# Performance work log

Measured on AMD Instinct MI355X. Metric: run time of the kernel, lower is better.

The kernel has to match this reference:

```python
import jax, jax.numpy as jnp
import numpy as np

K = 1_000_000      # number of sparse (2D-det, 3D-anchor) candidate pairs
ROWS = 200         # max 2D detections
COLS = 70400       # number of 3D anchors (200*176*2)
SENTINEL = -9999999.0


def setup_inputs() -> dict:
    key = jax.random.key(0)
    ks = jax.random.split(key, 12)
    input_1 = jax.random.normal(ks[0], (1, 4, 1, K), dtype=jnp.float32)
    idx0 = jax.random.randint(ks[1], (K,), 0, ROWS)
    idx1 = jax.random.randint(ks[2], (K,), 0, COLS)
    tensor_index = jnp.stack([idx0, idx1], axis=1).astype(jnp.int64)
    # fuse_2d_3d: 1x1 Conv2d stack 4->18->36->36->1 (weights as (out,in) matrices)
    def w(k, o, i):
        return jax.random.normal(k, (o, i), dtype=jnp.float32) * (1.0 / np.sqrt(i))
    return {
        "input_1": input_1,
        "tensor_index": tensor_index,
        "W1": w(ks[3], 18, 4),  "b1": jnp.zeros((18,), jnp.float32),
        "W2": w(ks[4], 36, 18), "b2": jnp.zeros((36,), jnp.float32),
        "W3": w(ks[5], 36, 36), "b3": jnp.zeros((36,), jnp.float32),
        "W4": w(ks[6], 1, 36),  "b4": jnp.zeros((1,), jnp.float32),
    }


def reference(input_1, tensor_index, W1, b1, W2, b2, W3, b3, W4, b4):
    # 1x1 convs over (1,4,1,K) are channel matmuls over the K pair axis.
    x = input_1[0, :, 0, :]                                   # (4, K)
    h = jax.nn.relu(jnp.dot(W1, x) + b1[:, None])             # (18, K)
    h = jax.nn.relu(jnp.dot(W2, h) + b2[:, None])             # (36, K)
    h = jax.nn.relu(jnp.dot(W3, h) + b3[:, None])             # (36, K)
    v = (jnp.dot(W4, h) + b4[:, None])[0]                     # (K,) fused score per pair
    # Scatter into dense sentinel-filled grid, then max-reduce the 200 dim
    # (equivalent to MaxPool2d([200,1]) in the original).
    dense = jnp.full((ROWS, COLS), SENTINEL, dtype=input_1.dtype)
    dense = dense.at[tensor_index[:, 0], tensor_index[:, 1]].max(v)
    out = jnp.max(dense, axis=0).reshape(1, -1, 1)            # (1, 70400, 1)
    flag = 1
    return (out, flag)
```

## Files before the change

### kernel.cpp

```cpp
#include <hip/hip_runtime.h>

#define KN 1000000
#define NCOLS 70400
#define NPAIRS (KN / 32)
#define NBLK 1024
#define NTHR 256

typedef _Float16 f16x8 __attribute__((ext_vector_type(8)));
typedef float    f32x4 __attribute__((ext_vector_type(4)));

__device__ __forceinline__ unsigned encodeF(float f) {
    unsigned b = __float_as_uint(f);
    return (b & 0x80000000u) ? ~b : (b | 0x80000000u);
}
__device__ __forceinline__ float decodeF(unsigned e) {
    unsigned b = (e & 0x80000000u) ? (e & 0x7fffffffu) : ~e;
    return __uint_as_float(b);
}
#define ENC_SENT 0x34E76980u

#define MFMA16(a, b, c) __builtin_amdgcn_mfma_f32_16x16x32_f16((a), (b), (c), 0, 0, 0)

#define OW1 0
#define OB1 72
#define OW2 90
#define OB2 738
#define OW3 774
#define OB3 2070
#define OW4 2106
#define OB4 2142
#define NWTS 2143


__global__ __launch_bounds__(NTHR)
__attribute__((amdgpu_waves_per_eu(4, 4)))
void mlp_scatter_mfma(const float* __restrict__ x, const int* __restrict__ tidx,
                      const float* __restrict__ W1, const float* __restrict__ b1,
                      const float* __restrict__ W2, const float* __restrict__ b2,
                      const float* __restrict__ W3, const float* __restrict__ b3,
                      const float* __restrict__ W4, const float* __restrict__ b4,
                      unsigned* __restrict__ outU)
{
    __shared__ float    sw[NWTS];
    __shared__ _Float16 smem[4][2][1152];

    const int t    = threadIdx.x;
    const int lane = t & 63;
    const int wv   = t >> 6;
    const int quad = lane >> 4;
    const int n    = lane & 15;

    for (int i = t; i < 72;   i += NTHR) sw[OW1 + i] = W1[i];
    for (int i = t; i < 18;   i += NTHR) sw[OB1 + i] = b1[i];
    for (int i = t; i < 648;  i += NTHR) sw[OW2 + i] = W2[i];
    for (int i = t; i < 36;   i += NTHR) sw[OB2 + i] = b2[i];
    for (int i = t; i < 1296; i += NTHR) sw[OW3 + i] = W3[i];
    for (int i = t; i < 36;   i += NTHR) sw[OB3 + i] = b3[i];
    for (int i = t; i < 36;   i += NTHR) sw[OW4 + i] = W4[i];
    if (t == 0) sw[OB4] = b4[0];

    _Float16* Ha = &smem[wv][0][0];
    _Float16* Hb = &smem[wv][1][0];

    for (int i = lane; i < 128; i += 64) {
        const int row = i >> 3, dc = i & 7;
        ((unsigned*)(Ha + row * 72 + 48))[dc] = 0u;
        ((unsigned*)(Hb + row * 72 + 48))[dc] = 0u;
    }
    __syncthreads();

    auto bf = [&](int off, int OUT, int IN, int tt, int ks) {
        f16x8 r;
#pragma unroll
        for (int j = 0; j < 8; ++j) {
            int k  = ks * 32 + quad * 8 + j;
            int ng = tt * 16 + n;
            float w = (ng < OUT && k < IN) ? sw[off + ng * IN + k] : 0.0f;
            r[j] = (_Float16)w;
        }
        return r;
    };
    const f16x8 B1_0 = bf(OW1, 18,  4, 0, 0), B1_1 = bf(OW1, 18,  4, 1, 0);
    const f16x8 B2_0 = bf(OW2, 36, 18, 0, 0), B2_1 = bf(OW2, 36, 18, 1, 0), B2_2 = bf(OW2, 36, 18, 2, 0);
    const f16x8 B3_00 = bf(OW3, 36, 36, 0, 0), B3_01 = bf(OW3, 36, 36, 0, 1);
    const f16x8 B3_10 = bf(OW3, 36, 36, 1, 0), B3_11 = bf(OW3, 36, 36, 1, 1);
    const f16x8 B3_20 = bf(OW3, 36, 36, 2, 0), B3_21 = bf(OW3, 36, 36, 2, 1);

    const float bias1_0 = sw[OB1 + n];
    const float bias1_1 = (n < 2) ? sw[OB1 + 16 + n] : 0.0f;
    const float bias2_0 = sw[OB2 + n], bias2_1 = sw[OB2 + 16 + n];
    const float bias2_2 = (n < 4) ? sw[OB2 + 32 + n] : 0.0f;
    const float bias3_0 = sw[OB3 + n], bias3_1 = sw[OB3 + 16 + n];
    const float bias3_2 = (n < 4) ? sw[OB3 + 32 + n] : 0.0f;
    const float b4s = sw[OB4];
    const float w4_0 = sw[OW4 + n], w4_1 = sw[OW4 + 16 + n];
    const float w4_2 = (n < 4) ? sw[OW4 + 32 + n] : 0.0f;

    const int gw = (blockIdx.x * blockDim.x + t) >> 6;
    const int nw = (gridDim.x * blockDim.x) >> 6;

    float cxa0, cxa1, cxa2, cxa3, cxb0, cxb1, cxb2, cxb3;
    int cca = 0, ccb = 0;
    if (gw < NPAIRS) {
        const int kb = gw * 32;
        cxa0 = x[0 * KN + kb + n];      cxb0 = x[0 * KN + kb + 16 + n];
        cxa1 = x[1 * KN + kb + n];      cxb1 = x[1 * KN + kb + 16 + n];
        cxa2 = x[2 * KN + kb + n];      cxb2 = x[2 * KN + kb + 16 + n];
        cxa3 = x[3 * KN + kb + n];      cxb3 = x[3 * KN + kb + 16 + n];
        cca  = tidx[2 * (kb + n) + 1];  ccb  = tidx[2 * (kb + 16 + n) + 1];
    }

    for (int p = gw; p < NPAIRS; ) {
        const int pn = p + nw;
        const float xa0 = cxa0, xa1 = cxa1, xa2 = cxa2, xa3 = cxa3;
        const float xb0 = cxb0, xb1 = cxb1, xb2 = cxb2, xb3 = cxb3;
        const int cola = cca, colb = ccb;
        if (pn < NPAIRS) {
            const int kb = pn * 32;
            cxa0 = x[0 * KN + kb + n];      cxb0 = x[0 * KN + kb + 16 + n];
            cxa1 = x[1 * KN + kb + n];      cxb1 = x[1 * KN + kb + 16 + n];
            cxa2 = x[2 * KN + kb + n];      cxb2 = x[2 * KN + kb + 16 + n];
            cxa3 = x[3 * KN + kb + n];      cxb3 = x[3 * KN + kb + 16 + n];
            cca  = tidx[2 * (kb + n) + 1];  ccb  = tidx[2 * (kb + 16 + n) + 1];
        }

        f16x8 a1a = {}, a1b = {};
        if (quad == 0) {
            a1a[0] = (_Float16)xa0; a1a[1] = (_Float16)xa1;
            a1a[2] = (_Float16)xa2; a1a[3] = (_Float16)xa3;
            a1b[0] = (_Float16)xb0; a1b[1] = (_Float16)xb1;
            a1b[2] = (_Float16)xb2; a1b[3] = (_Float16)xb3;
        }
        f32x4 c0a = {bias1_0, bias1_0, bias1_0, bias1_0};
        f32x4 c1a = {bias1_1, bias1_1, bias1_1, bias1_1};
        f32x4 c0b = c0a, c1b = c1a;
        c0a = MFMA16(a1a, B1_0, c0a);  c0b = MFMA16(a1b, B1_0, c0b);
        c1a = MFMA16(a1a, B1_1, c1a);  c1b = MFMA16(a1b, B1_1, c1b);
#pragma unroll
        for (int r = 0; r < 4; ++r) {
            const int row = (quad * 4 + r) * 72;
            Ha[row + n]      = (_Float16)fmaxf(c0a[r], 0.0f);
            Ha[row + 16 + n] = (_Float16)fmaxf(c1a[r], 0.0f);
            Hb[row + n]      = (_Float16)fmaxf(c0b[r], 0.0f);
            Hb[row + 16 + n] = (_Float16)fmaxf(c1b[r], 0.0f);
        }

        const f16x8 a2a = *(const f16x8*)&Ha[n * 72 + quad * 8];
        const f16x8 a2b = *(const f16x8*)&Hb[n * 72 + quad * 8];
        f32x4 d0a = {bias2_0, bias2_0, bias2_0, bias2_0};
        f32x4 d1a = {bias2_1, bias2_1, bias2_1, bias2_1};
        f32x4 d2a = {bias2_2, bias2_2, bias2_2, bias2_2};
        f32x4 d0b = d0a, d1b = d1a, d2b = d2a;
        d0a = MFMA16(a2a, B2_0, d0a);  d0b = MFMA16(a2b, B2_0, d0b);
        d1a = MFMA16(a2a, B2_1, d1a);  d1b = MFMA16(a2b, B2_1, d1b);
        d2a = MFMA16(a2a, B2_2, d2a);  d2b = MFMA16(a2b, B2_2, d2b);
#pragma unroll
        for (int r = 0; r < 4; ++r) {
            const int row = (quad * 4 + r) * 72;
            Ha[row + n]      = (_Float16)fmaxf(d0a[r], 0.0f);
            Ha[row + 16 + n] = (_Float16)fmaxf(d1a[r], 0.0f);
            Ha[row + 32 + n] = (_Float16)fmaxf(d2a[r], 0.0f);
            Hb[row + n]      = (_Float16)fmaxf(d0b[r], 0.0f);
            Hb[row + 16 + n] = (_Float16)fmaxf(d1b[r], 0.0f);
            Hb[row + 32 + n] = (_Float16)fmaxf(d2b[r], 0.0f);
        }

        const f16x8 a30a = *(const f16x8*)&Ha[n * 72 + quad * 8];
        const f16x8 a31a = *(const f16x8*)&Ha[n * 72 + 32 + quad * 8];
        const f16x8 a30b = *(const f16x8*)&Hb[n * 72 + quad * 8];
        const f16x8 a31b = *(const f16x8*)&Hb[n * 72 + 32 + quad * 8];
        f32x4 e0a = {bias3_0, bias3_0, bias3_0, bias3_0};
        f32x4 e1a = {bias3_1, bias3_1, bias3_1, bias3_1};
        f32x4 e2a = {bias3_2, bias3_2, bias3_2, bias3_2};
        f32x4 e0b = e0a, e1b = e1a, e2b = e2a;
        e0a = MFMA16(a30a, B3_00, e0a);  e0a = MFMA16(a31a, B3_01, e0a);
        e1a = MFMA16(a30a, B3_10, e1a);  e1a = MFMA16(a31a, B3_11, e1a);
        e2a = MFMA16(a30a, B3_20, e2a);  e2a = MFMA16(a31a, B3_21, e2a);
        e0b = MFMA16(a30b, B3_00, e0b);  e0b = MFMA16(a31b, B3_01, e0b);
        e1b = MFMA16(a30b, B3_10, e1b);  e1b = MFMA16(a31b, B3_11, e1b);
        e2b = MFMA16(a30b, B3_20, e2b);  e2b = MFMA16(a31b, B3_21, e2b);

        float pa[4], pb[4];
#pragma unroll
        for (int r = 0; r < 4; ++r) {
            pa[r] = fmaf(w4_0, fmaxf(e0a[r], 0.0f),
                    fmaf(w4_1, fmaxf(e1a[r], 0.0f),
                         w4_2 * fmaxf(e2a[r], 0.0f)));
            pb[r] = fmaf(w4_0, fmaxf(e0b[r], 0.0f),
                    fmaf(w4_1, fmaxf(e1b[r], 0.0f),
                         w4_2 * fmaxf(e2b[r], 0.0f)));
        }
#pragma unroll
        for (int m = 8; m >= 1; m >>= 1) {
#pragma unroll
            for (int r = 0; r < 4; ++r) {
                pa[r] += __shfl_xor(pa[r], m, 16);
                pb[r] += __shfl_xor(pb[r], m, 16);
            }
        }
        if ((n >> 2) == quad) {
            const int r = n & 3;
            atomicMax(&outU[cola], encodeF(pa[r] + b4s) - ENC_SENT);
            atomicMax(&outU[colb], encodeF(pb[r] + b4s) - ENC_SENT);
        }

        p = pn;
    }
}

__global__ __launch_bounds__(256) void init_kernel(unsigned* __restrict__ outU) {
    int gid = blockIdx.x * blockDim.x + threadIdx.x;
    if (gid < NCOLS) outU[gid] = 0u;
}

__global__ __launch_bounds__(256) void decode_kernel(unsigned* __restrict__ outU,
                                                     int out_size) {
    int gid = blockIdx.x * blockDim.x + threadIdx.x;
    if (gid < out_size) {
        float r = (gid < NCOLS) ? decodeF(outU[gid] + ENC_SENT) : 1.0f;
        ((float*)outU)[gid] = r;
    }
}

extern "C" void kernel_launch(void* const* d_in, const int* in_sizes, int n_in,
                              void* d_out, int out_size, void* d_ws, size_t ws_size,
                              hipStream_t stream) {
    const float* x    = (const float*)d_in[0];
    const int*   tidx = (const int*)d_in[1];
    const float* W1 = (const float*)d_in[2];
    const float* b1 = (const float*)d_in[3];
    const float* W2 = (const float*)d_in[4];
    const float* b2 = (const float*)d_in[5];
    const float* W3 = (const float*)d_in[6];
    const float* b3 = (const float*)d_in[7];
    const float* W4 = (const float*)d_in[8];
    const float* b4 = (const float*)d_in[9];
    unsigned* outU = (unsigned*)d_out;

    init_kernel<<<(NCOLS + 255) / 256, 256, 0, stream>>>(outU);

    mlp_scatter_mfma<<<NBLK, NTHR, 0, stream>>>(
        x, tidx, W1, b1, W2, b2, W3, b3, W4, b4, outU);

    decode_kernel<<<(out_size + 255) / 256, 256, 0, stream>>>(outU, out_size);
}
```

Before: 137.4 us.

## Privatize atomic max output into multiple workspace replicas reduced in decode

Each wave now scatters its atomicMax results into one of up to eight replicated copies of the output array held in workspace, chosen by wave index, and the decode kernel max-reduces across those replicas. This is meant to spread contention on the same columns across separate addresses and lower atomic serialization in L2. In exchange, init must zero eight times as much memory, decode reads eight arrays, and the atomic traffic becomes less cache-local. If the workspace is too small, it falls back to a single copy.

```diff
diff --git a/kernel.cpp b/kernel.cpp
--- a/kernel.cpp
+++ b/kernel.cpp
@@ -5,6 +5,7 @@
 #define NPAIRS (KN / 32)
 #define NBLK 1024
 #define NTHR 256
+#define NREP_MAX 8
 
 typedef _Float16 f16x8 __attribute__((ext_vector_type(8)));
 typedef float    f32x4 __attribute__((ext_vector_type(4)));
@@ -39,7 +40,7 @@
                       const float* __restrict__ W2, const float* __restrict__ b2,
                       const float* __restrict__ W3, const float* __restrict__ b3,
                       const float* __restrict__ W4, const float* __restrict__ b4,
-                      unsigned* __restrict__ outU)
+                      unsigned* __restrict__ rep, int rmask)
 {
     __shared__ float    sw[NWTS];
     __shared__ _Float16 smem[4][2][1152];
@@ -98,6 +99,8 @@
 
     const int gw = (blockIdx.x * blockDim.x + t) >> 6;
     const int nw = (gridDim.x * blockDim.x) >> 6;
+
+    unsigned* __restrict__ dst = rep + (size_t)(gw & rmask) * NCOLS;
 
     float cxa0, cxa1, cxa2, cxa3, cxb0, cxb1, cxb2, cxb3;
     int cca = 0, ccb = 0;
@@ -200,25 +203,36 @@
         }
         if ((n >> 2) == quad) {
             const int r = n & 3;
-            atomicMax(&outU[cola], encodeF(pa[r] + b4s) - ENC_SENT);
-            atomicMax(&outU[colb], encodeF(pb[r] + b4s) - ENC_SENT);
+            atomicMax(&dst[cola], encodeF(pa[r] + b4s) - ENC_SENT);
+            atomicMax(&dst[colb], encodeF(pb[r] + b4s) - ENC_SENT);
         }
 
         p = pn;
     }
 }
 
-__global__ __launch_bounds__(256) void init_kernel(unsigned* __restrict__ outU) {
+__global__ __launch_bounds__(256) void init_kernel(unsigned* __restrict__ rep,
+                                                   int total) {
     int gid = blockIdx.x * blockDim.x + threadIdx.x;
-    if (gid < NCOLS) outU[gid] = 0u;
-}
-
-__global__ __launch_bounds__(256) void decode_kernel(unsigned* __restrict__ outU,
+    if (gid < total) rep[gid] = 0u;
+}
+
+__global__ __launch_bounds__(256) void decode_kernel(const unsigned* __restrict__ rep,
+                                                     int nrep,
+                                                     float* __restrict__ out,
                                                      int out_size) {
     int gid = blockIdx.x * blockDim.x + threadIdx.x;
     if (gid < out_size) {
-        float r = (gid < NCOLS) ? decodeF(outU[gid] + ENC_SENT) : 1.0f;
-        ((float*)outU)[gid] = r;
+        float r = 1.0f;
+        if (gid < NCOLS) {
+            unsigned m = rep[gid];
+            for (int i = 1; i < nrep; ++i) {
+                unsigned v = rep[(size_t)i * NCOLS + gid];
+                m = (v > m) ? v : m;
+            }
+            r = decodeF(m + ENC_SENT);
+        }
+        out[gid] = r;
     }
 }
 
@@ -235,12 +249,23 @@
     const float* b3 = (const float*)d_in[7];
     const float* W4 = (const float*)d_in[8];
     const float* b4 = (const float*)d_in[9];
-    unsigned* outU = (unsigned*)d_out;
-
-    init_kernel<<<(NCOLS + 255) / 256, 256, 0, stream>>>(outU);
+
+    int nrep = 1;
+    unsigned* rep = (unsigned*)d_out;
+    if (d_ws && ws_size >= (size_t)NREP_MAX * NCOLS * sizeof(unsigned)) {
+        nrep = NREP_MAX;
+        rep  = (unsigned*)d_ws;
+    } else if (d_ws && ws_size >= (size_t)NCOLS * sizeof(unsigned)) {
+        nrep = 1;
+        rep  = (unsigned*)d_ws;
+    }
+    const int total = nrep * NCOLS;
+
+    init_kernel<<<(total + 255) / 256, 256, 0, stream>>>(rep, total);
 
     mlp_scatter_mfma<<<NBLK, NTHR, 0, stream>>>(
-        x, tidx, W1, b1, W2, b2, W3, b3, W4, b4, outU);
-
-    decode_kernel<<<(out_size + 255) / 256, 256, 0, stream>>>(outU, out_size);
-}
+        x, tidx, W1, b1, W2, b2, W3, b3, W4, b4, rep, nrep - 1);
+
+    decode_kernel<<<(out_size + 255) / 256, 256, 0, stream>>>(
+        rep, nrep, (float*)d_out, out_size);
+}
```

New measurement: 136.6 us. About the same (-0.6%).

## Privatize scatter-max atomics into per-XCC replicas with workgroup-scope atomics

Applied to the files above, without the earlier changes.

Each block reads its XCC ID from a hardware register and does its atomic max into a private replica of the output grid. Using workgroup memory scope lets each XCC's L2 handle the atomics instead of making them coherent across all XCCs. The init kernel now zeroes 16 replicas, and the decode kernel max-reduces across them before decoding. This adds extra init and reduction memory traffic. Correctness relies on blocks from different XCCs never sharing a replica, and on kernel boundaries making the L2 writes visible.

```diff
diff --git a/kernel.cpp b/kernel.cpp
--- a/kernel.cpp
+++ b/kernel.cpp
@@ -5,6 +5,7 @@
 #define NPAIRS (KN / 32)
 #define NBLK 1024
 #define NTHR 256
+#define NREP 16
 
 typedef _Float16 f16x8 __attribute__((ext_vector_type(8)));
 typedef float    f32x4 __attribute__((ext_vector_type(4)));
@@ -32,14 +33,15 @@
 #define NWTS 2143
 
 
+__device__ unsigned g_rep[NREP * NCOLS];
+
 __global__ __launch_bounds__(NTHR)
 __attribute__((amdgpu_waves_per_eu(4, 4)))
 void mlp_scatter_mfma(const float* __restrict__ x, const int* __restrict__ tidx,
                       const float* __restrict__ W1, const float* __restrict__ b1,
                       const float* __restrict__ W2, const float* __restrict__ b2,
                       const float* __restrict__ W3, const float* __restrict__ b3,
-                      const float* __restrict__ W4, const float* __restrict__ b4,
-                      unsigned* __restrict__ outU)
+                      const float* __restrict__ W4, const float* __restrict__ b4)
 {
     __shared__ float    sw[NWTS];
     __shared__ _Float16 smem[4][2][1152];
@@ -95,6 +97,10 @@
     const float b4s = sw[OB4];
     const float w4_0 = sw[OW4 + n], w4_1 = sw[OW4 + 16 + n];
     const float w4_2 = (n < 4) ? sw[OW4 + 32 + n] : 0.0f;
+
+    unsigned xcc;
+    asm volatile("s_getreg_b32 %0, hwreg(HW_REG_XCC_ID)" : "=s"(xcc));
+    unsigned* __restrict__ dst = g_rep + (size_t)(xcc & (NREP - 1)) * NCOLS;
 
     const int gw = (blockIdx.x * blockDim.x + t) >> 6;
     const int nw = (gridDim.x * blockDim.x) >> 6;
@@ -200,25 +206,38 @@
         }
         if ((n >> 2) == quad) {
             const int r = n & 3;
-            atomicMax(&outU[cola], encodeF(pa[r] + b4s) - ENC_SENT);
-            atomicMax(&outU[colb], encodeF(pb[r] + b4s) - ENC_SENT);
+            const unsigned ea = encodeF(pa[r] + b4s) - ENC_SENT;
+            const unsigned eb = encodeF(pb[r] + b4s) - ENC_SENT;
+            __hip_atomic_fetch_max(&dst[cola], ea, __ATOMIC_RELAXED,
+                                   __HIP_MEMORY_SCOPE_WORKGROUP);
+            __hip_atomic_fetch_max(&dst[colb], eb, __ATOMIC_RELAXED,
+                                   __HIP_MEMORY_SCOPE_WORKGROUP);
         }
 
         p = pn;
     }
 }
 
-__global__ __launch_bounds__(256) void init_kernel(unsigned* __restrict__ outU) {
+__global__ __launch_bounds__(256) void init_kernel() {
     int gid = blockIdx.x * blockDim.x + threadIdx.x;
-    if (gid < NCOLS) outU[gid] = 0u;
-}
-
-__global__ __launch_bounds__(256) void decode_kernel(unsigned* __restrict__ outU,
+    if (gid < NREP * NCOLS) g_rep[gid] = 0u;
+}
+
+__global__ __launch_bounds__(256) void decode_kernel(float* __restrict__ out,
                                                      int out_size) {
     int gid = blockIdx.x * blockDim.x + threadIdx.x;
     if (gid < out_size) {
-        float r = (gid < NCOLS) ? decodeF(outU[gid] + ENC_SENT) : 1.0f;
-        ((float*)outU)[gid] = r;
+        float r = 1.0f;
+        if (gid < NCOLS) {
+            unsigned m = g_rep[gid];
+#pragma unroll
+            for (int i = 1; i < NREP; ++i) {
+                unsigned v = g_rep[i * NCOLS + gid];
+                m = (v > m) ? v : m;
+            }
+            r = decodeF(m + ENC_SENT);
+        }
+        out[gid] = r;
     }
 }
 
@@ -235,12 +254,12 @@
     const float* b3 = (const float*)d_in[7];
     const float* W4 = (const float*)d_in[8];
     const float* b4 = (const float*)d_in[9];
-    unsigned* outU = (unsigned*)d_out;
-
-    init_kernel<<<(NCOLS + 255) / 256, 256, 0, stream>>>(outU);
+
+    init_kernel<<<(NREP * NCOLS + 255) / 256, 256, 0, stream>>>();
 
     mlp_scatter_mfma<<<NBLK, NTHR, 0, stream>>>(
-        x, tidx, W1, b1, W2, b2, W3, b3, W4, b4, outU);
-
-    decode_kernel<<<(out_size + 255) / 256, 256, 0, stream>>>(outU, out_size);
-}
+        x, tidx, W1, b1, W2, b2, W3, b3, W4, b4);
+
+    decode_kernel<<<(out_size + 255) / 256, 256, 0, stream>>>(
+        (float*)d_out, out_size);
+}
```

Measured after the change: 141.6 us. 3.0% more time.

## Keep MLP activations in registers via transposed 16x16x16 MFMA chaining

Applied to the files above, without the earlier changes.

Reformulates each layer as W·H so the MFMA output layout (rows across quads, columns across lanes) directly matches the next layer's B-operand layout. This removes the per-layer LDS round trip (stores, reloads and the padded shared buffers) in favour of register-resident f16 conversions. The final dot product now needs only two cross-quad shuffles instead of four rounds of 16-lane shuffles. The smaller 16x16x16 MFMA needs more instructions per layer, and the waves_per_eu attribute is dropped, which may change register allocation and occupancy.

```diff
diff --git a/kernel.cpp b/kernel.cpp
--- a/kernel.cpp
+++ b/kernel.cpp
@@ -6,8 +6,10 @@
 #define NBLK 1024
 #define NTHR 256
 
-typedef _Float16 f16x8 __attribute__((ext_vector_type(8)));
+typedef _Float16 f16x4 __attribute__((ext_vector_type(4)));
 typedef float    f32x4 __attribute__((ext_vector_type(4)));
+
+#define MFMA16(a, b, c) __builtin_amdgcn_mfma_f32_16x16x16f16((a), (b), (c), 0, 0, 0)
 
 __device__ __forceinline__ unsigned encodeF(float f) {
     unsigned b = __float_as_uint(f);
@@ -18,8 +20,6 @@
     return __uint_as_float(b);
 }
 #define ENC_SENT 0x34E76980u
-
-#define MFMA16(a, b, c) __builtin_amdgcn_mfma_f32_16x16x32_f16((a), (b), (c), 0, 0, 0)
 
 #define OW1 0
 #define OB1 72
@@ -33,7 +33,6 @@
 
 
 __global__ __launch_bounds__(NTHR)
-__attribute__((amdgpu_waves_per_eu(4, 4)))
 void mlp_scatter_mfma(const float* __restrict__ x, const int* __restrict__ tidx,
                       const float* __restrict__ W1, const float* __restrict__ b1,
                       const float* __restrict__ W2, const float* __restrict__ b2,
@@ -41,12 +40,10 @@
                       const float* __restrict__ W4, const float* __restrict__ b4,
                       unsigned* __restrict__ outU)
 {
-    __shared__ float    sw[NWTS];
-    __shared__ _Float16 smem[4][2][1152];
+    __shared__ float sw[NWTS];
 
     const int t    = threadIdx.x;
     const int lane = t & 63;
-    const int wv   = t >> 6;
     const int quad = lane >> 4;
     const int n    = lane & 15;
 
@@ -58,43 +55,42 @@
     for (int i = t; i < 36;   i += NTHR) sw[OB3 + i] = b3[i];
     for (int i = t; i < 36;   i += NTHR) sw[OW4 + i] = W4[i];
     if (t == 0) sw[OB4] = b4[0];
-
-    _Float16* Ha = &smem[wv][0][0];
-    _Float16* Hb = &smem[wv][1][0];
-
-    for (int i = lane; i < 128; i += 64) {
-        const int row = i >> 3, dc = i & 7;
-        ((unsigned*)(Ha + row * 72 + 48))[dc] = 0u;
-        ((unsigned*)(Hb + row * 72 + 48))[dc] = 0u;
-    }
     __syncthreads();
 
-    auto bf = [&](int off, int OUT, int IN, int tt, int ks) {
-        f16x8 r;
-#pragma unroll
-        for (int j = 0; j < 8; ++j) {
-            int k  = ks * 32 + quad * 8 + j;
-            int ng = tt * 16 + n;
-            float w = (ng < OUT && k < IN) ? sw[off + ng * IN + k] : 0.0f;
+    auto af = [&](int off, int OUT, int IN, int tt, int s) {
+        f16x4 r;
+#pragma unroll
+        for (int j = 0; j < 4; ++j) {
+            const int m = tt * 16 + n;
+            const int k = s * 16 + quad * 4 + j;
+            const float w = (m < OUT && k < IN) ? sw[off + m * IN + k] : 0.0f;
             r[j] = (_Float16)w;
         }
         return r;
     };
-    const f16x8 B1_0 = bf(OW1, 18,  4, 0, 0), B1_1 = bf(OW1, 18,  4, 1, 0);
-    const f16x8 B2_0 = bf(OW2, 36, 18, 0, 0), B2_1 = bf(OW2, 36, 18, 1, 0), B2_2 = bf(OW2, 36, 18, 2, 0);
-    const f16x8 B3_00 = bf(OW3, 36, 36, 0, 0), B3_01 = bf(OW3, 36, 36, 0, 1);
-    const f16x8 B3_10 = bf(OW3, 36, 36, 1, 0), B3_11 = bf(OW3, 36, 36, 1, 1);
-    const f16x8 B3_20 = bf(OW3, 36, 36, 2, 0), B3_21 = bf(OW3, 36, 36, 2, 1);
-
-    const float bias1_0 = sw[OB1 + n];
-    const float bias1_1 = (n < 2) ? sw[OB1 + 16 + n] : 0.0f;
-    const float bias2_0 = sw[OB2 + n], bias2_1 = sw[OB2 + 16 + n];
-    const float bias2_2 = (n < 4) ? sw[OB2 + 32 + n] : 0.0f;
-    const float bias3_0 = sw[OB3 + n], bias3_1 = sw[OB3 + 16 + n];
-    const float bias3_2 = (n < 4) ? sw[OB3 + 32 + n] : 0.0f;
-    const float b4s = sw[OB4];
-    const float w4_0 = sw[OW4 + n], w4_1 = sw[OW4 + 16 + n];
-    const float w4_2 = (n < 4) ? sw[OW4 + 32 + n] : 0.0f;
+    auto bv = [&](int off, int OUT, int tt) {
+        f32x4 c;
+#pragma unroll
+        for (int r = 0; r < 4; ++r) {
+            const int m = tt * 16 + quad * 4 + r;
+            c[r] = (m < OUT) ? sw[off + m] : 0.0f;
+        }
+        return c;
+    };
+
+    const f16x4 A1_0  = af(OW1, 18,  4, 0, 0), A1_1  = af(OW1, 18,  4, 1, 0);
+    const f16x4 A2_00 = af(OW2, 36, 18, 0, 0), A2_01 = af(OW2, 36, 18, 0, 1);
+    const f16x4 A2_10 = af(OW2, 36, 18, 1, 0), A2_11 = af(OW2, 36, 18, 1, 1);
+    const f16x4 A2_20 = af(OW2, 36, 18, 2, 0), A2_21 = af(OW2, 36, 18, 2, 1);
+    const f16x4 A3_00 = af(OW3, 36, 36, 0, 0), A3_01 = af(OW3, 36, 36, 0, 1), A3_02 = af(OW3, 36, 36, 0, 2);
+    const f16x4 A3_10 = af(OW3, 36, 36, 1, 0), A3_11 = af(OW3, 36, 36, 1, 1), A3_12 = af(OW3, 36, 36, 1, 2);
+    const f16x4 A3_20 = af(OW3, 36, 36, 2, 0), A3_21 = af(OW3, 36, 36, 2, 1), A3_22 = af(OW3, 36, 36, 2, 2);
+
+    const f32x4 C1_0 = bv(OB1, 18, 0), C1_1 = bv(OB1, 18, 1);
+    const f32x4 C2_0 = bv(OB2, 36, 0), C2_1 = bv(OB2, 36, 1), C2_2 = bv(OB2, 36, 2);
+    const f32x4 C3_0 = bv(OB3, 36, 0), C3_1 = bv(OB3, 36, 1), C3_2 = bv(OB3, 36, 2);
+    const f32x4 V4_0 = bv(OW4, 36, 0), V4_1 = bv(OW4, 36, 1), V4_2 = bv(OW4, 36, 2);
+    const float b4s  = sw[OB4];
 
     const int gw = (blockIdx.x * blockDim.x + t) >> 6;
     const int nw = (gridDim.x * blockDim.x) >> 6;
@@ -109,6 +105,13 @@
         cxa3 = x[3 * KN + kb + n];      cxb3 = x[3 * KN + kb + 16 + n];
         cca  = tidx[2 * (kb + n) + 1];  ccb  = tidx[2 * (kb + 16 + n) + 1];
     }
+
+    auto rl = [](f32x4 v) {
+        f16x4 h;
+#pragma unroll
+        for (int r = 0; r < 4; ++r) h[r] = (_Float16)fmaxf(v[r], 0.0f);
+        return h;
+    };
 
     for (int p = gw; p < NPAIRS; ) {
         const int pn = p + nw;
@@ -124,85 +127,58 @@
             cca  = tidx[2 * (kb + n) + 1];  ccb  = tidx[2 * (kb + 16 + n) + 1];
         }
 
-        f16x8 a1a = {}, a1b = {};
+        f16x4 B0a = {}, B0b = {};
         if (quad == 0) {
-            a1a[0] = (_Float16)xa0; a1a[1] = (_Float16)xa1;
-            a1a[2] = (_Float16)xa2; a1a[3] = (_Float16)xa3;
-            a1b[0] = (_Float16)xb0; a1b[1] = (_Float16)xb1;
-            a1b[2] = (_Float16)xb2; a1b[3] = (_Float16)xb3;
-        }
-        f32x4 c0a = {bias1_0, bias1_0, bias1_0, bias1_0};
-        f32x4 c1a = {bias1_1, bias1_1, bias1_1, bias1_1};
-        f32x4 c0b = c0a, c1b = c1a;
-        c0a = MFMA16(a1a, B1_0, c0a);  c0b = MFMA16(a1b, B1_0, c0b);
-        c1a = MFMA16(a1a, B1_1, c1a);  c1b = MFMA16(a1b, B1_1, c1b);
+            B0a[0] = (_Float16)xa0; B0a[1] = (_Float16)xa1;
+            B0a[2] = (_Float16)xa2; B0a[3] = (_Float16)xa3;
+            B0b[0] = (_Float16)xb0; B0b[1] = (_Float16)xb1;
+            B0b[2] = (_Float16)xb2; B0b[3] = (_Float16)xb3;
+        }
+
+        f32x4 d1a0 = MFMA16(A1_0, B0a, C1_0);
+        f32x4 d1b0 = MFMA16(A1_0, B0b, C1_0);
+        f32x4 d1a1 = MFMA16(A1_1, B0a, C1_1);
+        f32x4 d1b1 = MFMA16(A1_1, B0b, C1_1);
+        const f16x4 B1a0 = rl(d1a0), B1a1 = rl(d1a1);
+        const f16x4 B1b0 = rl(d1b0), B1b1 = rl(d1b1);
+
+        f32x4 d2a0 = MFMA16(A2_00, B1a0, C2_0);  d2a0 = MFMA16(A2_01, B1a1, d2a0);
+        f32x4 d2b0 = MFMA16(A2_00, B1b0, C2_0);  d2b0 = MFMA16(A2_01, B1b1, d2b0);
+        f32x4 d2a1 = MFMA16(A2_10, B1a0, C2_1);  d2a1 = MFMA16(A2_11, B1a1, d2a1);
+        f32x4 d2b1 = MFMA16(A2_10, B1b0, C2_1);  d2b1 = MFMA16(A2_11, B1b1, d2b1);
+        f32x4 d2a2 = MFMA16(A2_20, B1a0, C2_2);  d2a2 = MFMA16(A2_21, B1a1, d2a2);
+        f32x4 d2b2 = MFMA16(A2_20, B1b0, C2_2);  d2b2 = MFMA16(A2_21, B1b1, d2b2);
+        const f16x4 B2a0 = rl(d2a0), B2a1 = rl(d2a1), B2a2 = rl(d2a2);
+        const f16x4 B2b0 = rl(d2b0), B2b1 = rl(d2b1), B2b2 = rl(d2b2);
+
+        f32x4 d3a0 = MFMA16(A3_00, B2a0, C3_0);
+        d3a0 = MFMA16(A3_01, B2a1, d3a0);  d3a0 = MFMA16(A3_02, B2a2, d3a0);
+        f32x4 d3b0 = MFMA16(A3_00, B2b0, C3_0);
+        d3b0 = MFMA16(A3_01, B2b1, d3b0);  d3b0 = MFMA16(A3_02, B2b2, d3b0);
+        f32x4 d3a1 = MFMA16(A3_10, B2a0, C3_1);
+        d3a1 = MFMA16(A3_11, B2a1, d3a1);  d3a1 = MFMA16(A3_12, B2a2, d3a1);
+        f32x4 d3b1 = MFMA16(A3_10, B2b0, C3_1);
+        d3b1 = MFMA16(A3_11, B2b1, d3b1);  d3b1 = MFMA16(A3_12, B2b2, d3b1);
+        f32x4 d3a2 = MFMA16(A3_20, B2a0, C3_2);
+        d3a2 = MFMA16(A3_21, B2a1, d3a2);  d3a2 = MFMA16(A3_22, B2a2, d3a2);
+        f32x4 d3b2 = MFMA16(A3_20, B2b0, C3_2);
+        d3b2 = MFMA16(A3_21, B2b1, d3b2);  d3b2 = MFMA16(A3_22, B2b2, d3b2);
+
+        float pa = 0.0f, pb = 0.0f;
 #pragma unroll
         for (int r = 0; r < 4; ++r) {
-            const int row = (quad * 4 + r) * 72;
-            Ha[row + n]      = (_Float16)fmaxf(c0a[r], 0.0f);
-            Ha[row + 16 + n] = (_Float16)fmaxf(c1a[r], 0.0f);
-            Hb[row + n]      = (_Float16)fmaxf(c0b[r], 0.0f);
-            Hb[row + 16 + n] = (_Float16)fmaxf(c1b[r], 0.0f);
-        }
-
-        const f16x8 a2a = *(const f16x8*)&Ha[n * 72 + quad * 8];
-        const f16x8 a2b = *(const f16x8*)&Hb[n * 72 + quad * 8];
-        f32x4 d0a = {bias2_0, bias2_0, bias2_0, bias2_0};
-        f32x4 d1a = {bias2_1, bias2_1, bias2_1, bias2_1};
-        f32x4 d2a = {bias2_2, bias2_2, bias2_2, bias2_2};
-        f32x4 d0b = d0a, d1b = d1a, d2b = d2a;
-        d0a = MFMA16(a2a, B2_0, d0a);  d0b = MFMA16(a2b, B2_0, d0b);
-        d1a = MFMA16(a2a, B2_1, d1a);  d1b = MFMA16(a2b, B2_1, d1b);
-        d2a = MFMA16(a2a, B2_2, d2a);  d2b = MFMA16(a2b, B2_2, d2b);
-#pragma unroll
-        for (int r = 0; r < 4; ++r) {
-            const int row = (quad * 4 + r) * 72;
-            Ha[row + n]      = (_Float16)fmaxf(d0a[r], 0.0f);
-            Ha[row + 16 + n] = (_Float16)fmaxf(d1a[r], 0.0f);
-            Ha[row + 32 + n] = (_Float16)fmaxf(d2a[r], 0.0f);
-            Hb[row + n]      = (_Float16)fmaxf(d0b[r], 0.0f);
-            Hb[row + 16 + n] = (_Float16)fmaxf(d1b[r], 0.0f);
-            Hb[row + 32 + n] = (_Float16)fmaxf(d2b[r], 0.0f);
-        }
-
-        const f16x8 a30a = *(const f16x8*)&Ha[n * 72 + quad * 8];
-        const f16x8 a31a = *(const f16x8*)&Ha[n * 72 + 32 + quad * 8];
-        const f16x8 a30b = *(const f16x8*)&Hb[n * 72 + quad * 8];
-        const f16x8 a31b = *(const f16x8*)&Hb[n * 72 + 32 + quad * 8];
-        f32x4 e0a = {bias3_0, bias3_0, bias3_0, bias3_0};
-        f32x4 e1a = {bias3_1, bias3_1, bias3_1, bias3_1};
-        f32x4 e2a = {bias3_2, bias3_2, bias3_2, bias3_2};
-        f32x4 e0b = e0a, e1b = e1a, e2b = e2a;
-        e0a = MFMA16(a30a, B3_00, e0a);  e0a = MFMA16(a31a, B3_01, e0a);
-        e1a = MFMA16(a30a, B3_10, e1a);  e1a = MFMA16(a31a, B3_11, e1a);
-        e2a = MFMA16(a30a, B3_20, e2a);  e2a = MFMA16(a31a, B3_21, e2a);
-        e0b = MFMA16(a30b, B3_00, e0b);  e0b = MFMA16(a31b, B3_01, e0b);
-        e1b = MFMA16(a30b, B3_10, e1b);  e1b = MFMA16(a31b, B3_11, e1b);
-        e2b = MFMA16(a30b, B3_20, e2b);  e2b = MFMA16(a31b, B3_21, e2b);
-
-        float pa[4], pb[4];
-#pragma unroll
-        for (int r = 0; r < 4; ++r) {
-            pa[r] = fmaf(w4_0, fmaxf(e0a[r], 0.0f),
-                    fmaf(w4_1, fmaxf(e1a[r], 0.0f),
-                         w4_2 * fmaxf(e2a[r], 0.0f)));
-            pb[r] = fmaf(w4_0, fmaxf(e0b[r], 0.0f),
-                    fmaf(w4_1, fmaxf(e1b[r], 0.0f),
-                         w4_2 * fmaxf(e2b[r], 0.0f)));
-        }
-#pragma unroll
-        for (int m = 8; m >= 1; m >>= 1) {
-#pragma unroll
-            for (int r = 0; r < 4; ++r) {
-                pa[r] += __shfl_xor(pa[r], m, 16);
-                pb[r] += __shfl_xor(pb[r], m, 16);
-            }
-        }
-        if ((n >> 2) == quad) {
-            const int r = n & 3;
-            atomicMax(&outU[cola], encodeF(pa[r] + b4s) - ENC_SENT);
-            atomicMax(&outU[colb], encodeF(pb[r] + b4s) - ENC_SENT);
-        }
+            pa = fmaf(V4_0[r], fmaxf(d3a0[r], 0.0f), pa);
+            pa = fmaf(V4_1[r], fmaxf(d3a1[r], 0.0f), pa);
+            pa = fmaf(V4_2[r], fmaxf(d3a2[r], 0.0f), pa);
+            pb = fmaf(V4_0[r], fmaxf(d3b0[r], 0.0f), pb);
+            pb = fmaf(V4_1[r], fmaxf(d3b1[r], 0.0f), pb);
+            pb = fmaf(V4_2[r], fmaxf(d3b2[r], 0.0f), pb);
+        }
+        pa += __shfl_xor(pa, 16);  pa += __shfl_xor(pa, 32);
+        pb += __shfl_xor(pb, 16);  pb += __shfl_xor(pb, 32);
+
+        if (quad == 0)      atomicMax(&outU[cola], encodeF(pa + b4s) - ENC_SENT);
+        else if (quad == 1) atomicMax(&outU[colb], encodeF(pb + b4s) - ENC_SENT);
 
         p = pn;
     }
```

After: 136.0 us. No clear change (-1.0%).
